# Kernel optimization log

Hardware: AMD Instinct MI355X
Metric: run time of the kernel (lower is better)

Reference implementation:

```python
import jax, jax.numpy as jnp
import numpy as np

N, E, D, A = 50000, 1_600_000, 32, 2
H1, C1, H2, C2 = 4, 16, 2, 32  # GATv2Conv(D,16,heads=4) -> 64; GATv2Conv(64,32,heads=2) -> 64


def setup_inputs() -> dict:
    key = jax.random.key(0)
    ks = jax.random.split(key, 16)

    def glorot(k, shape):
        fan = shape[0] + shape[-1]
        return jax.random.normal(k, shape, jnp.float32) * np.float32(np.sqrt(2.0 / fan))

    return {
        "x": jax.random.normal(ks[0], (N, D), jnp.float32),
        "edge_index": jax.random.randint(ks[1], (2, E), 0, N),
        "edge_attr": jax.random.normal(ks[2], (E, 2), jnp.float32),
        # GATv2 layer 1 (lin_l/lin_r with bias, lin_edge no bias, att [H,C], out bias)
        "w1_l": glorot(ks[3], (D, H1 * C1)), "b1_l": jnp.zeros((H1 * C1,), jnp.float32),
        "w1_r": glorot(ks[4], (D, H1 * C1)), "b1_r": jnp.zeros((H1 * C1,), jnp.float32),
        "w1_e": glorot(ks[5], (2, H1 * C1)),
        "att1": glorot(ks[6], (H1, C1)),
        "bias1": jnp.zeros((H1 * C1,), jnp.float32),
        # GATv2 layer 2
        "w2_l": glorot(ks[7], (H1 * C1, H2 * C2)), "b2_l": jnp.zeros((H2 * C2,), jnp.float32),
        "w2_r": glorot(ks[8], (H1 * C1, H2 * C2)), "b2_r": jnp.zeros((H2 * C2,), jnp.float32),
        "w2_e": glorot(ks[9], (2, H2 * C2)),
        "att2": glorot(ks[10], (H2, C2)),
        "bias2": jnp.zeros((H2 * C2,), jnp.float32),
        # heads
        "w_actor": glorot(ks[11], (H2 * C2, A)), "b_actor": jnp.zeros((A,), jnp.float32),
        "w_critic": glorot(ks[12], (H2 * C2, 1)), "b_critic": jnp.zeros((1,), jnp.float32),
        "log_std": jnp.zeros((A,), jnp.float32),
    }


def _gatv2(x, src, dst, eattr, Wl, bl, Wr, br, We, att, bias, H, C, n):
    # PyG GATv2Conv: message j->i with i = dst, j = src
    xl = (x @ Wl + bl).reshape(n, H, C)  # source-side transform (x_j)
    xr = (x @ Wr + br).reshape(n, H, C)  # target-side transform (x_i)
    ee = (eattr @ We).reshape(-1, H, C)  # per-edge embedding
    z = jax.nn.leaky_relu(xl[src] + xr[dst] + ee, 0.2)  # [Etot, H, C]
    logits = jnp.einsum('ehc,hc->eh', z, att)  # [Etot, H]
    # segment softmax over incoming edges of each dst node
    m = jax.ops.segment_max(logits, dst, num_segments=n)
    p = jnp.exp(logits - m[dst])
    denom = jax.ops.segment_sum(p, dst, num_segments=n)
    alpha = p / denom[dst]  # every node has a self-loop -> denom > 0
    msg = xl[src] * alpha[:, :, None]  # [Etot, H, C]
    out = jax.ops.segment_sum(msg, dst, num_segments=n)
    return out.reshape(n, H * C) + bias


def reference(x, edge_index, edge_attr,
              w1_l, b1_l, w1_r, b1_r, w1_e, att1, bias1,
              w2_l, b2_l, w2_r, b2_r, w2_e, att2, bias2,
              w_actor, b_actor, w_critic, b_critic, log_std):
    src, dst = edge_index[0], edge_index[1]
    # add_self_loops=True, fill_value='mean': self-loop edge_attr = mean of incoming edge_attr
    cnt = jax.ops.segment_sum(jnp.ones((edge_attr.shape[0],), x.dtype), dst, num_segments=N)
    sums = jax.ops.segment_sum(edge_attr, dst, num_segments=N)
    loop_attr = sums / jnp.maximum(cnt, 1.0)[:, None]
    loop = jnp.arange(N, dtype=src.dtype)
    src_f = jnp.concatenate([src, loop])
    dst_f = jnp.concatenate([dst, loop])
    ea = jnp.concatenate([edge_attr, loop_attr], axis=0)

    h = jax.nn.relu(_gatv2(x, src_f, dst_f, ea, w1_l, b1_l, w1_r, b1_r, w1_e, att1, bias1, H1, C1, N))
    h = jax.nn.relu(_gatv2(h, src_f, dst_f, ea, w2_l, b2_l, w2_r, b2_r, w2_e, att2, bias2, H2, C2, N))

    action_mean = jnp.tanh(h @ w_actor + b_actor)  # [N, A]
    value = h @ w_critic + b_critic               # [N, 1]
    std = jnp.exp(log_std)                        # [A]  (Normal(action_mean, std))
    return action_mean, std, value
```

## Files before the change

kernel.cpp:

```cpp
#include <hip/hip_runtime.h>
#include <hip/hip_fp16.h>
#include <math.h>

#define DIN   32
#define F1    64
#define F2    64

typedef __attribute__((ext_vector_type(2))) float f32x2;

__device__ __forceinline__ f32x2 pkfma(f32x2 a, f32x2 b, f32x2 c) {
#if __has_builtin(__builtin_elementwise_fma)
    return __builtin_elementwise_fma(a, b, c);
#else
    return a * b + c;
#endif
}
__device__ __forceinline__ f32x2 pkmax(f32x2 a, f32x2 b) {
    f32x2 r; r.x = fmaxf(a.x, b.x); r.y = fmaxf(a.y, b.y); return r;
}

__device__ __forceinline__ unsigned bf16pack(float a, float b) {
    unsigned ua = __float_as_uint(a);
    unsigned ub = __float_as_uint(b);
    ua = (ua + 0x7FFFu + ((ua >> 16) & 1u)) >> 16;
    ub = (ub + 0x7FFFu + ((ub >> 16) & 1u)) >> 16;
    return ua | (ub << 16);
}

template <int K>
__device__ __forceinline__ void lin_lr_body(int bid,
        const float* __restrict__ x,
        const float* __restrict__ Wl, const float* __restrict__ bl,
        const float* __restrict__ Wr, const float* __restrict__ br,
        __half* __restrict__ xl, float* __restrict__ xr, int n) {
    __shared__ float Ash[32][K + 4];
    __shared__ float Wsh[K][128];
    const int t = threadIdx.x;
    const int node0 = bid * 32;

    for (int idx = t; idx < 32 * (K / 4); idx += 256) {
        int m = idx / (K / 4), kq = idx % (K / 4);
        float4 v = make_float4(0.f, 0.f, 0.f, 0.f);
        if (node0 + m < n) v = ((const float4*)(x + (size_t)(node0 + m) * K))[kq];
        *(float4*)&Ash[m][kq * 4] = v;
    }
    for (int idx = t; idx < K * 32; idx += 256) {
        int k = idx / 32, j4 = idx % 32;
        float4 v = (j4 < 16) ? ((const float4*)(Wl + (size_t)k * 64))[j4]
                             : ((const float4*)(Wr + (size_t)k * 64))[j4 - 16];
        *(float4*)&Wsh[k][j4 * 4] = v;
    }
    __syncthreads();

    const int ty = t >> 4;
    const int tx = t & 15;
    f32x2 c0[4], c1[4];
#pragma unroll
    for (int j = 0; j < 4; j++) {
        c0[j].x = 0.f; c0[j].y = 0.f;
        c1[j].x = 0.f; c1[j].y = 0.f;
    }

#pragma unroll 4
    for (int k = 0; k < K; k++) {
        float a0 = Ash[ty * 2 + 0][k];
        float a1 = Ash[ty * 2 + 1][k];
        float4 w0 = *(const float4*)&Wsh[k][tx * 8];
        float4 w1 = *(const float4*)&Wsh[k][tx * 8 + 4];
        f32x2 wv0; wv0.x = w0.x; wv0.y = w0.y;
        f32x2 wv1; wv1.x = w0.z; wv1.y = w0.w;
        f32x2 wv2; wv2.x = w1.x; wv2.y = w1.y;
        f32x2 wv3; wv3.x = w1.z; wv3.y = w1.w;
        f32x2 a0s; a0s.x = a0; a0s.y = a0;
        f32x2 a1s; a1s.x = a1; a1s.y = a1;
        c0[0] = pkfma(a0s, wv0, c0[0]);
        c0[1] = pkfma(a0s, wv1, c0[1]);
        c0[2] = pkfma(a0s, wv2, c0[2]);
        c0[3] = pkfma(a0s, wv3, c0[3]);
        c1[0] = pkfma(a1s, wv0, c1[0]);
        c1[1] = pkfma(a1s, wv1, c1[1]);
        c1[2] = pkfma(a1s, wv2, c1[2]);
        c1[3] = pkfma(a1s, wv3, c1[3]);
    }

    const float* bsrc = (tx < 8) ? bl : br;
    int jb = (tx < 8) ? tx * 8 : (tx - 8) * 8;
    float4 b0 = ((const float4*)(bsrc + jb))[0];
    float4 b1 = ((const float4*)(bsrc + jb))[1];
#pragma unroll
    for (int m = 0; m < 2; m++) {
        int node = node0 + ty * 2 + m;
        if (node >= n) continue;
        const f32x2* cc = (m == 0) ? c0 : c1;
        float o0 = cc[0].x + b0.x, o1 = cc[0].y + b0.y;
        float o2 = cc[1].x + b0.z, o3 = cc[1].y + b0.w;
        float o4 = cc[2].x + b1.x, o5 = cc[2].y + b1.y;
        float o6 = cc[3].x + b1.z, o7 = cc[3].y + b1.w;
        if (tx < 8) {
            __half2 h0 = __floats2half2_rn(o0, o1);
            __half2 h1 = __floats2half2_rn(o2, o3);
            __half2 h2 = __floats2half2_rn(o4, o5);
            __half2 h3 = __floats2half2_rn(o6, o7);
            uint4 pk;
            pk.x = *(unsigned*)&h0; pk.y = *(unsigned*)&h1;
            pk.z = *(unsigned*)&h2; pk.w = *(unsigned*)&h3;
            *((uint4*)(xl + (size_t)node * 64 + jb)) = pk;
        } else {
            float4 f0 = make_float4(o0, o1, o2, o3);
            float4 f1 = make_float4(o4, o5, o6, o7);
            ((float4*)(xr + (size_t)node * 64 + jb))[0] = f0;
            ((float4*)(xr + (size_t)node * 64 + jb))[1] = f1;
        }
    }
}

__global__ __launch_bounds__(512, 2)
void count_scatter(const int* __restrict__ srcr, const int* __restrict__ dstr,
                   const float* __restrict__ ea, int* __restrict__ cursor,
                   int2* __restrict__ inter, int E, int Ec, int NB, int cap) {
    __shared__ int2 recsh[3584];
    __shared__ unsigned short rksh[3584];
    __shared__ unsigned char bksh[3584];
    __shared__ int hist[256];
    __shared__ int colsh[256];
    const int blk = blockIdx.x;
    const int t = threadIdx.x;
    if (t < 256) hist[t] = 0;
    __syncthreads();
    const int s0 = blk * Ec, s1 = min(E, s0 + Ec);
    const int cnt = s1 - s0;
    for (int e = s0 + t; e < s1; e += 512) {
        int d = dstr[e];
        float2 v = ((const float2*)ea)[e];
        int2 r;
        r.x = srcr[e] | ((d & 255) << 24);
        r.y = (int)bf16pack(v.x, v.y);
        int li = e - s0;
        int bk = (unsigned)d >> 8;
        recsh[li] = r;
        bksh[li] = (unsigned char)bk;
        rksh[li] = (unsigned short)atomicAdd(&hist[bk], 1);
    }
    __syncthreads();
    if (t < NB) {
        int h = hist[t];
        colsh[t] = t * cap + (h ? atomicAdd(&cursor[t], h) : 0);
    }
    __syncthreads();
    for (int li = t; li < cnt; li += 512)
        inter[colsh[bksh[li]] + (int)rksh[li]] = recsh[li];
}

__global__ __launch_bounds__(256, 2)
void fused_csr_lin1(const int2* __restrict__ inter, const int* __restrict__ cursor,
                    int2* __restrict__ rse, int2* __restrict__ edges,
                    int NB, int N, int cap,
                    const float* __restrict__ x,
                    const float* __restrict__ Wl, const float* __restrict__ bl,
                    const float* __restrict__ Wr, const float* __restrict__ br,
                    __half* __restrict__ xl, float* __restrict__ xr, int n) {
    if ((int)blockIdx.x >= NB) {
        lin_lr_body<DIN>(blockIdx.x - NB, x, Wl, bl, Wr, br, xl, xr, n);
        return;
    }
    __shared__ int sh[256];
    __shared__ int cur[256];
    const int b = blockIdx.x, t = threadIdx.x;
    const int bstart = b * cap;
    const int bend = bstart + cursor[b];

    sh[t] = 0;
    __syncthreads();
    for (int pos = bstart + t; pos < bend; pos += 256)
        atomicAdd(&sh[((unsigned)inter[pos].x) >> 24], 1);
    __syncthreads();
    int cnt_v = sh[t];
    __syncthreads();
    sh[t] = cnt_v;
    __syncthreads();
    for (int off = 1; off < 256; off <<= 1) {
        int xv = (t >= off) ? sh[t - off] : 0;
        __syncthreads();
        sh[t] += xv;
        __syncthreads();
    }
    {
        int excl = sh[t] - cnt_v;
        cur[t] = excl;
        int myrs = bstart + excl;
        int node = b * 256 + t;
        if (node < N) rse[node] = make_int2(myrs, myrs + cnt_v);
    }
    __syncthreads();
    for (int pos = bstart + t; pos < bend; pos += 256) {
        int2 r = inter[pos];
        int k = atomicAdd(&cur[((unsigned)r.x) >> 24], 1);
        r.x &= 0x00FFFFFF;
        edges[bstart + k] = r;
    }
    int zend = (b + 1) * cap + ((b == NB - 1) ? 64 : 0);
    for (int pos = bend + t; pos < zend; pos += 256)
        edges[pos] = make_int2(0, 0);
}

__global__ __launch_bounds__(256, 2)
void lin_lr_tiled64(const float* __restrict__ x,
                    const float* __restrict__ Wl, const float* __restrict__ bl,
                    const float* __restrict__ Wr, const float* __restrict__ br,
                    __half* __restrict__ xl, float* __restrict__ xr, int n) {
    lin_lr_body<F1>(blockIdx.x, x, Wl, bl, Wr, br, xl, xr, n);
}

template <int H, int C, bool FUSE_HEADS>
__global__ __launch_bounds__(256)
void gat_kernel(const __half* __restrict__ xl, const float* __restrict__ xr,
                const int2* __restrict__ rse,
                const int2* __restrict__ edges,
                const float* __restrict__ We, const float* __restrict__ att,
                const float* __restrict__ bias, float* __restrict__ hout,
                const float* __restrict__ wa, const float* __restrict__ ba,
                const float* __restrict__ wc, const float* __restrict__ bc,
                const float* __restrict__ ls, float* __restrict__ pout,
                int n) {
    constexpr int LPH = C / 4;
    if (FUSE_HEADS && blockIdx.x == 0 && threadIdx.x < 2)
        pout[(size_t)n * 2 + threadIdx.x] = expf(ls[threadIdx.x]);
    const int lane = threadIdx.x & 63;
    const int wid = (blockIdx.x * blockDim.x + threadIdx.x) >> 6;
    if (wid >= n) return;
    const int i = wid;
    const int g = lane >> 4;
    const int q = lane & 15;

    const uint2* xlh = (const uint2*)xl;
    const float4 xri4 = ((const float4*)(xr + (size_t)i * 64))[q];
    const float4 we04 = ((const float4*)We)[q];
    const float4 we14 = ((const float4*)(We + 64))[q];
    const float4 av4 = ((const float4*)att)[q];
    const float LOG2E = 1.4426950408889634f;
    f32x2 xrlo; xrlo.x = xri4.x; xrlo.y = xri4.y;
    f32x2 xrhi; xrhi.x = xri4.z; xrhi.y = xri4.w;
    f32x2 we0lo; we0lo.x = we04.x; we0lo.y = we04.y;
    f32x2 we0hi; we0hi.x = we04.z; we0hi.y = we04.w;
    f32x2 we1lo; we1lo.x = we14.x; we1lo.y = we14.y;
    f32x2 we1hi; we1hi.x = we14.z; we1hi.y = we14.w;
    f32x2 avlo; avlo.x = av4.x * LOG2E; avlo.y = av4.y * LOG2E;
    f32x2 avhi; avhi.x = av4.z * LOG2E; avhi.y = av4.w * LOG2E;

    auto h4lo = [](uint2 h) -> f32x2 {
        float2 a = __half22float2(*(__half2*)&h.x);
        f32x2 r; r.x = a.x; r.y = a.y; return r;
    };
    auto h4hi = [](uint2 h) -> f32x2 {
        float2 b = __half22float2(*(__half2*)&h.y);
        f32x2 r; r.x = b.x; r.y = b.y; return r;
    };
    auto logit_of = [&](f32x2 xlo, f32x2 xhi, float ea0, float ea1) -> float {
        f32x2 e0; e0.x = ea0; e0.y = ea0;
        f32x2 e1; e1.x = ea1; e1.y = ea1;
        f32x2 ylo = xlo + pkfma(e0, we0lo, pkfma(e1, we1lo, xrlo));
        f32x2 yhi = xhi + pkfma(e0, we0hi, pkfma(e1, we1hi, xrhi));
        ylo = pkmax(ylo, ylo * 0.2f);
        yhi = pkmax(yhi, yhi * 0.2f);
        f32x2 l2 = pkfma(ylo, avlo, yhi * avhi);
        return l2.x + l2.y;
    };

    float den = 0.f;
    float sea0 = 0.f, sea1 = 0.f;
    f32x2 aclo; aclo.x = 0.f; aclo.y = 0.f;
    f32x2 achi; achi.x = 0.f; achi.y = 0.f;

    const int2 se = rse[i];
    const int e0 = se.x, e1 = se.y;
    const int r = (e1 - e0) & 7;

    if (r) {
        int2 h0 = edges[e0 + g];
        int2 h1 = edges[e0 + 4 + g];
        uint2 u0 = xlh[(h0.x << 4) + q];
        uint2 u1 = xlh[(h1.x << 4) + q];
        f32x2 x0lo = h4lo(u0), x0hi = h4hi(u0);
        f32x2 x1lo = h4lo(u1), x1hi = h4hi(u1);
        const bool v0 = g < r;
        const bool v1 = (4 + g) < r;
        float ea00 = v0 ? __int_as_float(h0.y << 16) : 0.f;
        float ea01 = v0 ? __int_as_float(h0.y & 0xFFFF0000) : 0.f;
        float ea10 = v1 ? __int_as_float(h1.y << 16) : 0.f;
        float ea11 = v1 ? __int_as_float(h1.y & 0xFFFF0000) : 0.f;
        sea0 += ea00 + ea10;
        sea1 += ea01 + ea11;
        float l0 = logit_of(x0lo, x0hi, ea00, ea01);
        float l1 = logit_of(x1lo, x1hi, ea10, ea11);
#pragma unroll
        for (int m = 1; m < LPH; m <<= 1) {
            l0 += __shfl_xor(l0, m, 64);
            l1 += __shfl_xor(l1, m, 64);
        }
        float p0 = v0 ? exp2f(l0) : 0.f;
        float p1 = v1 ? exp2f(l1) : 0.f;
        den += p0 + p1;
        f32x2 p0s; p0s.x = p0; p0s.y = p0;
        f32x2 p1s; p1s.x = p1; p1s.y = p1;
        aclo = pkfma(p0s, x0lo, pkfma(p1s, x1lo, aclo));
        achi = pkfma(p0s, x0hi, pkfma(p1s, x1hi, achi));
    }

    const int em = e0 + r;
    int2 rn0 = edges[em + g];
    int2 rn1 = edges[em + 4 + g];
    uint2 xpn0 = xlh[(rn0.x << 4) + q];
    uint2 xpn1 = xlh[(rn1.x << 4) + q];

    for (int eb = em; eb < e1; eb += 8) {
        int2 r0 = rn0, r1 = rn1;
        f32x2 x0lo = h4lo(xpn0), x0hi = h4hi(xpn0);
        f32x2 x1lo = h4lo(xpn1), x1hi = h4hi(xpn1);
        rn0 = edges[eb + 8 + g];
        rn1 = edges[eb + 12 + g];
        xpn0 = xlh[(rn0.x << 4) + q];
        xpn1 = xlh[(rn1.x << 4) + q];

        float ea00 = __int_as_float(r0.y << 16);
        float ea01 = __int_as_float(r0.y & 0xFFFF0000);
        float ea10 = __int_as_float(r1.y << 16);
        float ea11 = __int_as_float(r1.y & 0xFFFF0000);
        sea0 += ea00 + ea10;
        sea1 += ea01 + ea11;

        float l0 = logit_of(x0lo, x0hi, ea00, ea01);
        float l1 = logit_of(x1lo, x1hi, ea10, ea11);
#pragma unroll
        for (int m = 1; m < LPH; m <<= 1) {
            l0 += __shfl_xor(l0, m, 64);
            l1 += __shfl_xor(l1, m, 64);
        }
        float p0 = exp2f(l0);
        float p1 = exp2f(l1);
        den += p0 + p1;
        f32x2 p0s; p0s.x = p0; p0s.y = p0;
        f32x2 p1s; p1s.x = p1; p1s.y = p1;
        aclo = pkfma(p0s, x0lo, pkfma(p1s, x1lo, aclo));
        achi = pkfma(p0s, x0hi, pkfma(p1s, x1hi, achi));
    }

    float a0 = aclo.x, a1 = aclo.y, a2 = achi.x, a3 = achi.y;

#pragma unroll
    for (int m = 16; m < 64; m <<= 1) {
        den += __shfl_xor(den, m, 64);
        a0 += __shfl_xor(a0, m, 64);
        a1 += __shfl_xor(a1, m, 64);
        a2 += __shfl_xor(a2, m, 64);
        a3 += __shfl_xor(a3, m, 64);
        sea0 += __shfl_xor(sea0, m, 64);
        sea1 += __shfl_xor(sea1, m, 64);
    }

    const int cnt_i = e1 - e0;
    const float invc = cnt_i ? 1.0f / (float)cnt_i : 0.f;
    const float lamx = sea0 * invc;
    const float lamy = sea1 * invc;
    uint2 us = xlh[(i << 4) + q];
    f32x2 xslo = h4lo(us), xshi = h4hi(us);
    {
        float l = logit_of(xslo, xshi, lamx, lamy);
#pragma unroll
        for (int m = 1; m < LPH; m <<= 1) l += __shfl_xor(l, m, 64);
        float p = exp2f(l);
        den += p;
        a0 = fmaf(p, xslo.x, a0);
        a1 = fmaf(p, xslo.y, a1);
        a2 = fmaf(p, xshi.x, a2);
        a3 = fmaf(p, xshi.y, a3);
    }

    float rd = 1.0f / den;
    const float4 bv = ((const float4*)bias)[q];
    float4 o;
    o.x = fmaxf(fmaf(a0, rd, bv.x), 0.f);
    o.y = fmaxf(fmaf(a1, rd, bv.y), 0.f);
    o.z = fmaxf(fmaf(a2, rd, bv.z), 0.f);
    o.w = fmaxf(fmaf(a3, rd, bv.w), 0.f);

    if (!FUSE_HEADS) {
        if (g == 0) ((float4*)(hout + (size_t)i * 64))[q] = o;
    } else {
        float4 wa01 = ((const float4*)wa)[q * 2];
        float4 wa23 = ((const float4*)wa)[q * 2 + 1];
        float4 wcv  = ((const float4*)wc)[q];
        float d0 = o.x * wa01.x + o.y * wa01.z + o.z * wa23.x + o.w * wa23.z;
        float d1 = o.x * wa01.y + o.y * wa01.w + o.z * wa23.y + o.w * wa23.w;
        float d2 = o.x * wcv.x + o.y * wcv.y + o.z * wcv.z + o.w * wcv.w;
#pragma unroll
        for (int m = 1; m < 16; m <<= 1) {
            d0 += __shfl_xor(d0, m, 64);
            d1 += __shfl_xor(d1, m, 64);
            d2 += __shfl_xor(d2, m, 64);
        }
        if (lane == 0) {
            pout[(size_t)i * 2 + 0] = tanhf(d0 + ba[0]);
            pout[(size_t)i * 2 + 1] = tanhf(d1 + ba[1]);
            pout[(size_t)n * 2 + 2 + i] = d2 + bc[0];
        }
    }
}


extern "C" void kernel_launch(void* const* d_in, const int* in_sizes, int n_in,
                              void* d_out, int out_size, void* d_ws, size_t ws_size,
                              hipStream_t stream) {
    const float* x    = (const float*)d_in[0];
    const int*   ei   = (const int*)  d_in[1];
    const float* ea   = (const float*)d_in[2];
    const float* w1l  = (const float*)d_in[3];
    const float* b1l  = (const float*)d_in[4];
    const float* w1r  = (const float*)d_in[5];
    const float* b1r  = (const float*)d_in[6];
    const float* w1e  = (const float*)d_in[7];
    const float* att1 = (const float*)d_in[8];
    const float* bias1= (const float*)d_in[9];
    const float* w2l  = (const float*)d_in[10];
    const float* b2l  = (const float*)d_in[11];
    const float* w2r  = (const float*)d_in[12];
    const float* b2r  = (const float*)d_in[13];
    const float* w2e  = (const float*)d_in[14];
    const float* att2 = (const float*)d_in[15];
    const float* bias2= (const float*)d_in[16];
    const float* wa   = (const float*)d_in[17];
    const float* ba   = (const float*)d_in[18];
    const float* wc   = (const float*)d_in[19];
    const float* bc   = (const float*)d_in[20];
    const float* ls   = (const float*)d_in[21];

    const int N = in_sizes[0] / DIN;
    const int E = in_sizes[2] / 2;
    const int* srcr = ei;
    const int* dstr = ei + E;

    const int NB = (N + 255) >> 8;
    const int NCH = 512;
    const int Ec = (E + NCH - 1) / NCH;
    int cap = (E + NB - 1) / NB;
    cap = ((cap + cap / 4) + 63) & ~63;

    char* p = (char*)d_ws;
    auto alloc = [&](size_t bytes) -> void* {
        void* r = (void*)p;
        p += (bytes + 255) & ~(size_t)255;
        return r;
    };
    int*    cursor = (int*)   alloc(256 * 4);
    int2*   rse    = (int2*)  alloc((size_t)N * 8);
    int2*   edges  = (int2*)  alloc(((size_t)NB * cap + 64) * 8);
    __half* xl     = (__half*)alloc((size_t)N * F1 * 2);
    float*  xr     = (float*) alloc((size_t)N * F1 * 4);
    float*  h1     = (float*) alloc((size_t)N * F1 * 4);
    float*  h2     = (float*) alloc((size_t)N * F2 * 4);
    int2* inter = (int2*)h1;
    (void)ws_size; (void)n_in; (void)out_size;

    hipMemsetAsync(cursor, 0, 256 * 4, stream);

    const int TB = 256;
    int gridGemm = (N + 31) / 32;
    int gridWave = (N + 3) / 4;

    count_scatter<<<NCH, 512, 0, stream>>>(srcr, dstr, ea, cursor, inter,
                                           E, Ec, NB, cap);
    fused_csr_lin1<<<NB + gridGemm, TB, 0, stream>>>(
        inter, cursor, rse, edges, NB, N, cap,
        x, w1l, b1l, w1r, b1r, xl, xr, N);

    gat_kernel<4, 16, false><<<gridWave, TB, 0, stream>>>(
        xl, xr, rse, edges, w1e, att1, bias1, h1,
        nullptr, nullptr, nullptr, nullptr, nullptr, nullptr, N);
    lin_lr_tiled64<<<gridGemm, TB, 0, stream>>>(h1, w2l, b2l, w2r, b2r, xl, xr, N);
    gat_kernel<2, 32, true><<<gridWave, TB, 0, stream>>>(
        xl, xr, rse, edges, w2e, att2, bias2, h2,
        wa, ba, wc, bc, ls, (float*)d_out, N);
}
```

Baseline: 284.1 us.

## Fuse layer-2 linear transforms into the layer-1 GAT aggregation kernel epilogue

Removes the separate lin_lr_tiled64 launch by having each wave, after computing its node's layer-1 output, immediately compute xl2/xr2 for layer 2 with shuffles and per-lane weight loads. This avoids writing h1 to memory and reading it back, and drops one kernel launch. In exchange, each wave does a 64x64 matvec with weights read from global/L1 instead of a tiled GEMM with LDS reuse, which adds per-node ALU and load pressure inside the latency-bound gather kernel. Separate xl2/xr2 buffers are allocated so layer 1 inputs are not overwritten while being read.

```diff
diff --git a/kernel.cpp b/kernel.cpp
--- a/kernel.cpp
+++ b/kernel.cpp
@@ -203,21 +203,16 @@
         edges[pos] = make_int2(0, 0);
 }
 
-__global__ __launch_bounds__(256, 2)
-void lin_lr_tiled64(const float* __restrict__ x,
-                    const float* __restrict__ Wl, const float* __restrict__ bl,
-                    const float* __restrict__ Wr, const float* __restrict__ br,
-                    __half* __restrict__ xl, float* __restrict__ xr, int n) {
-    lin_lr_body<F1>(blockIdx.x, x, Wl, bl, Wr, br, xl, xr, n);
-}
-
-template <int H, int C, bool FUSE_HEADS>
+template <int H, int C, bool FUSE_HEADS, bool FUSE_LIN2>
 __global__ __launch_bounds__(256)
 void gat_kernel(const __half* __restrict__ xl, const float* __restrict__ xr,
                 const int2* __restrict__ rse,
                 const int2* __restrict__ edges,
                 const float* __restrict__ We, const float* __restrict__ att,
                 const float* __restrict__ bias, float* __restrict__ hout,
+                const float* __restrict__ w2l, const float* __restrict__ b2l,
+                const float* __restrict__ w2r, const float* __restrict__ b2r,
+                __half* __restrict__ xl2o, float* __restrict__ xr2o,
                 const float* __restrict__ wa, const float* __restrict__ ba,
                 const float* __restrict__ wc, const float* __restrict__ bc,
                 const float* __restrict__ ls, float* __restrict__ pout,
@@ -383,7 +378,30 @@
     o.z = fmaxf(fmaf(a2, rd, bv.z), 0.f);
     o.w = fmaxf(fmaf(a3, rd, bv.w), 0.f);
 
-    if (!FUSE_HEADS) {
+    if (FUSE_LIN2) {
+        const int hl = lane & 31;
+        const bool isl = lane < 32;
+        const float2* Wp = (const float2*)(isl ? w2l : w2r) + hl;
+        const float* bsel = isl ? b2l : b2r;
+        float s0 = 0.f, s1 = 0.f;
+#pragma unroll
+        for (int k = 0; k < 64; k++) {
+            float comp = ((k & 3) == 0) ? o.x : ((k & 3) == 1) ? o.y
+                       : ((k & 3) == 2) ? o.z : o.w;
+            float hk = __shfl(comp, k >> 2, 64);
+            float2 wv = Wp[k * 32];
+            s0 = fmaf(hk, wv.x, s0);
+            s1 = fmaf(hk, wv.y, s1);
+        }
+        s0 += bsel[2 * hl];
+        s1 += bsel[2 * hl + 1];
+        if (isl) {
+            __half2 hx = __floats2half2_rn(s0, s1);
+            *(unsigned*)(xl2o + (size_t)i * 64 + 2 * hl) = *(unsigned*)&hx;
+        } else {
+            ((float2*)(xr2o + (size_t)i * 64))[hl] = make_float2(s0, s1);
+        }
+    } else if (!FUSE_HEADS) {
         if (g == 0) ((float4*)(hout + (size_t)i * 64))[q] = o;
     } else {
         float4 wa01 = ((const float4*)wa)[q * 2];
@@ -455,9 +473,9 @@
     int2*   edges  = (int2*)  alloc(((size_t)NB * cap + 64) * 8);
     __half* xl     = (__half*)alloc((size_t)N * F1 * 2);
     float*  xr     = (float*) alloc((size_t)N * F1 * 4);
-    float*  h1     = (float*) alloc((size_t)N * F1 * 4);
-    float*  h2     = (float*) alloc((size_t)N * F2 * 4);
-    int2* inter = (int2*)h1;
+    __half* xl2    = (__half*)alloc((size_t)N * F2 * 2);
+    float*  xr2    = (float*) alloc((size_t)N * F2 * 4);
+    int2* inter = (int2*)xl2;
     (void)ws_size; (void)n_in; (void)out_size;
 
     hipMemsetAsync(cursor, 0, 256 * 4, stream);
@@ -472,11 +490,13 @@
         inter, cursor, rse, edges, NB, N, cap,
         x, w1l, b1l, w1r, b1r, xl, xr, N);
 
-    gat_kernel<4, 16, false><<<gridWave, TB, 0, stream>>>(
-        xl, xr, rse, edges, w1e, att1, bias1, h1,
+    gat_kernel<4, 16, false, true><<<gridWave, TB, 0, stream>>>(
+        xl, xr, rse, edges, w1e, att1, bias1, nullptr,
+        w2l, b2l, w2r, b2r, xl2, xr2,
         nullptr, nullptr, nullptr, nullptr, nullptr, nullptr, N);
-    lin_lr_tiled64<<<gridGemm, TB, 0, stream>>>(h1, w2l, b2l, w2r, b2r, xl, xr, N);
-    gat_kernel<2, 32, true><<<gridWave, TB, 0, stream>>>(
-        xl, xr, rse, edges, w2e, att2, bias2, h2,
+
+    gat_kernel<2, 32, true, false><<<gridWave, TB, 0, stream>>>(
+        xl2, xr2, rse, edges, w2e, att2, bias2, nullptr,
+        nullptr, nullptr, nullptr, nullptr, nullptr, nullptr,
         wa, ba, wc, bc, ls, (float*)d_out, N);
 }
```

Measured after the change: 336.1 us. 1.18x slower.
